# Optimization experiments

Measured on AMD Instinct MI355X. Metric: run time of the kernel, lower is better.

Reference implementation:

```python
import jax, jax.numpy as jnp
import numpy as np

N = 100_000   # nodes
E = 1_600_000 # edges (avg degree 16)
D = 64        # in_channel == out_channel (residual requires equality)
EPS = 1e-5    # BatchNorm1d eps


def setup_inputs() -> dict:
    key = jax.random.key(0)
    ks = jax.random.split(key, 8)
    x = jax.random.normal(ks[0], (N, D), dtype=jnp.float32)
    adj_val = jax.random.uniform(ks[1], (E,), dtype=jnp.float32) * 0.25  # sparse poly_adj values
    W = jax.random.normal(ks[2], (D, D), dtype=jnp.float32) / np.sqrt(D)  # Linear weight [out,in]
    b = jnp.zeros((D,), dtype=jnp.float32)
    gamma = jnp.ones((D,), dtype=jnp.float32)
    beta = jnp.zeros((D,), dtype=jnp.float32)
    adj_row = jax.random.randint(ks[3], (E,), 0, N, dtype=jnp.int32)
    adj_col = jax.random.randint(ks[4], (E,), 0, N, dtype=jnp.int32)
    return {"x": x, "adj_val": adj_val, "W": W, "b": b,
            "gamma": gamma, "beta": beta, "adj_row": adj_row, "adj_col": adj_col}


def reference(x, adj_val, W, b, gamma, beta, adj_row, adj_col):
    # h = poly_adj @ x  (COO SpMM via gather + segment_sum)
    h = jax.ops.segment_sum(adj_val[:, None] * x[adj_col], adj_row, num_segments=N)
    # Linear
    h = h @ W.T + b
    # residual
    h = h + x
    # BatchNorm1d (training-mode batch stats, biased variance)
    mean = jnp.mean(h, axis=0)
    var = jnp.mean(jnp.square(h - mean), axis=0)
    h = (h - mean) * jax.lax.rsqrt(var + EPS) * gamma + beta
    # ReLU (dropout with p=0 is identity)
    h = jax.nn.relu(h)
    return h
```

## Files before the change

### kernel.cpp

```cpp
#include <hip/hip_runtime.h>

#define DCH 64
#define BN_EPS 1e-5f

#define SUPSH 12
#define NSUPMAX 32
#define CAPS 67584
#define CHA 2048
#define CHB 2048
#define CPS 33
#define CAPF 1216
#define CITER 8

__device__ __forceinline__ unsigned bf16pair(float lo, float hi) {
    unsigned ul = (__float_as_uint(lo) + 0x8000u) >> 16;
    unsigned uh = (__float_as_uint(hi) + 0x8000u) & 0xffff0000u;
    return ul | uh;
}
__device__ __forceinline__ float bf_lo(unsigned u) { return __uint_as_float(u << 16); }
__device__ __forceinline__ float bf_hi(unsigned u) { return __uint_as_float(u & 0xffff0000u); }

__global__ __launch_bounds__(256) void gemm_xwt(const float* __restrict__ x,
                                                const float* __restrict__ W,
                                                unsigned short* __restrict__ yb,
                                                int* __restrict__ cursA,
                                                int* __restrict__ cursB,
                                                float* __restrict__ stats,
                                                int N) {
    const int tid = threadIdx.x;
    if (blockIdx.x == 0) {
        for (int i = tid; i < 2048; i += 256) cursB[i] = i * CAPF;
    } else if (blockIdx.x == 1) {
        if (tid < 128) stats[tid] = 0.f;
        if (tid < NSUPMAX) cursA[tid] = tid * CAPS;
    }

    __shared__ float xs[128 * 68];
    __shared__ float wt[64 * 64];
    const int blockRow = blockIdx.x * 128;

#pragma unroll
    for (int jj = 0; jj < 4; ++jj) {
        int idx4 = tid * 16 + jj * 4;
        int o = idx4 >> 6, k = idx4 & 63;
        float4 w4 = *(const float4*)&W[idx4];
        wt[(k + 0) * 64 + o] = w4.x;
        wt[(k + 1) * 64 + o] = w4.y;
        wt[(k + 2) * 64 + o] = w4.z;
        wt[(k + 3) * 64 + o] = w4.w;
    }
#pragma unroll
    for (int jj = 0; jj < 8; ++jj) {
        int f4 = tid + 256 * jj;
        int rl = f4 >> 4, k4 = (f4 & 15) * 4;
        int row = blockRow + rl;
        float4 v = make_float4(0.f, 0.f, 0.f, 0.f);
        if (row < N) v = *(const float4*)&x[row * DCH + k4];
        *(float4*)&xs[rl * 68 + k4] = v;
    }
    __syncthreads();

    const int tc = tid & 7;
    const int tr = tid >> 3;
    const int dc = tc * 8;
    float acc[4][8];
#pragma unroll
    for (int i = 0; i < 4; ++i)
#pragma unroll
        for (int j = 0; j < 8; ++j) acc[i][j] = 0.f;

    for (int k4 = 0; k4 < 16; ++k4) {
        float4 xv[4];
#pragma unroll
        for (int i = 0; i < 4; ++i)
            xv[i] = *(const float4*)&xs[(tr + 32 * i) * 68 + k4 * 4];
#pragma unroll
        for (int kk = 0; kk < 4; ++kk) {
            int k = k4 * 4 + kk;
            float4 w0 = *(const float4*)&wt[k * 64 + dc];
            float4 w1 = *(const float4*)&wt[k * 64 + dc + 4];
#pragma unroll
            for (int i = 0; i < 4; ++i) {
                float xvi = (kk == 0) ? xv[i].x : (kk == 1) ? xv[i].y
                           : (kk == 2) ? xv[i].z : xv[i].w;
                acc[i][0] = fmaf(xvi, w0.x, acc[i][0]);
                acc[i][1] = fmaf(xvi, w0.y, acc[i][1]);
                acc[i][2] = fmaf(xvi, w0.z, acc[i][2]);
                acc[i][3] = fmaf(xvi, w0.w, acc[i][3]);
                acc[i][4] = fmaf(xvi, w1.x, acc[i][4]);
                acc[i][5] = fmaf(xvi, w1.y, acc[i][5]);
                acc[i][6] = fmaf(xvi, w1.z, acc[i][6]);
                acc[i][7] = fmaf(xvi, w1.w, acc[i][7]);
            }
        }
    }
#pragma unroll
    for (int i = 0; i < 4; ++i) {
        int row = blockRow + tr + 32 * i;
        if (row < N) {
            uint4 p;
            p.x = bf16pair(acc[i][0], acc[i][1]);
            p.y = bf16pair(acc[i][2], acc[i][3]);
            p.z = bf16pair(acc[i][4], acc[i][5]);
            p.w = bf16pair(acc[i][6], acc[i][7]);
            *(uint4*)&yb[row * DCH + dc] = p;
        }
    }
}

__global__ __launch_bounds__(256) void bin_coarse(const int* __restrict__ rows,
                                                  const int* __restrict__ cols,
                                                  const float* __restrict__ vals,
                                                  int* __restrict__ cursA,
                                                  int2* __restrict__ edgesA,
                                                  int E, int NSUP) {
    __shared__ int2 stage[CHA];
    __shared__ unsigned char bOf[CHA];
    __shared__ int wc[32 * NSUPMAX];
    __shared__ int startB[NSUPMAX], totB[NSUPMAX], gbase[NSUPMAX];
    const int tid = threadIdx.x, lane = tid & 63, wave = tid >> 6;
    const int base = blockIdx.x * CHA;
    const int cnt = min(CHA, E - base);

    for (int i = tid; i < 32 * NSUPMAX; i += 256) wc[i] = 0;
    __syncthreads();

    int myr[CITER], myrank[CITER];
#pragma unroll
    for (int it = 0; it < CITER; ++it) {
        int k = tid + it * 256;
        bool act = k < cnt;
        int r = act ? rows[base + k] : 0;
        myr[it] = r;
        int key = r >> SUPSH;
        unsigned long long m = __ballot(act);
#pragma unroll
        for (int bit = 0; bit < 5; ++bit) {
            unsigned long long bb = __ballot((key >> bit) & 1);
            m &= ((key >> bit) & 1) ? bb : ~bb;
        }
        int rk = __popcll(m & ((1ULL << lane) - 1ULL));
        myrank[it] = rk;
        if (act && rk == 0) wc[(wave * CITER + it) * NSUPMAX + key] = __popcll(m);
    }
    __syncthreads();
    if (tid < NSUP) {
        int run = 0;
        for (int sub = 0; sub < 32; ++sub) {
            int t = wc[sub * NSUPMAX + tid];
            wc[sub * NSUPMAX + tid] = run;
            run += t;
        }
        totB[tid] = run;
    }
    __syncthreads();
    if (wave == 0) {
        int v = (lane < NSUP) ? totB[lane] : 0;
        int inc = v;
#pragma unroll
        for (int off = 1; off < 32; off <<= 1) {
            int u = __shfl_up(inc, off);
            if (lane >= off) inc += u;
        }
        if (lane < NSUP) {
            startB[lane] = inc - v;
            gbase[lane] = v ? atomicAdd(&cursA[lane], v) : 0;
        }
    }
    __syncthreads();
#pragma unroll
    for (int it = 0; it < CITER; ++it) {
        int k = tid + it * 256;
        if (k < cnt) {
            int r = myr[it];
            int key = r >> SUPSH;
            int pos = startB[key] + wc[(wave * CITER + it) * NSUPMAX + key] + myrank[it];
            int2 pk;
            pk.x = cols[base + k] | ((r & 4095) << 17);
            pk.y = __float_as_int(vals[base + k]);
            stage[pos] = pk;
            bOf[pos] = (unsigned char)key;
        }
    }
    __syncthreads();
#pragma unroll
    for (int it = 0; it < CITER; ++it) {
        int i = tid + it * 256;
        if (i < cnt) {
            int s = bOf[i];
            int pos = gbase[s] + (i - startB[s]);
            if (pos < (s + 1) * CAPS) edgesA[pos] = stage[i];
        }
    }
}

__global__ __launch_bounds__(256) void bin_fine(const int2* __restrict__ edgesA,
                                                const int* __restrict__ cursA,
                                                int* __restrict__ cursB,
                                                int2* __restrict__ edgesB) {
    __shared__ int2 stage[CHB];
    __shared__ unsigned char bOf[CHB];
    __shared__ int wc[32 * 64];
    __shared__ int startB[64], totB[64], gbase[64];
    const int tid = threadIdx.x, lane = tid & 63, wave = tid >> 6;
    const int s = blockIdx.x / CPS;
    const int c = blockIdx.x % CPS;
    const int base = s * CAPS + c * CHB;
    int fill = min(cursA[s] - s * CAPS, CAPS);
    int cnt = fill - c * CHB;
    cnt = max(0, min(CHB, cnt));

    for (int i = tid; i < 32 * 64; i += 256) wc[i] = 0;
    __syncthreads();

    int2 mypk[CITER];
    int myrank[CITER];
#pragma unroll
    for (int it = 0; it < CITER; ++it) {
        int k = tid + it * 256;
        bool act = k < cnt;
        int2 p = act ? edgesA[base + k] : make_int2(0, 0);
        mypk[it] = p;
        int key = (p.x >> 23) & 63;
        unsigned long long m = __ballot(act);
#pragma unroll
        for (int bit = 0; bit < 6; ++bit) {
            unsigned long long bb = __ballot((key >> bit) & 1);
            m &= ((key >> bit) & 1) ? bb : ~bb;
        }
        int rk = __popcll(m & ((1ULL << lane) - 1ULL));
        myrank[it] = rk;
        if (act && rk == 0) wc[(wave * CITER + it) * 64 + key] = __popcll(m);
    }
    __syncthreads();
    if (tid < 64) {
        int run = 0;
        for (int sub = 0; sub < 32; ++sub) {
            int t = wc[sub * 64 + tid];
            wc[sub * 64 + tid] = run;
            run += t;
        }
        totB[tid] = run;
    }
    __syncthreads();
    if (wave == 0) {
        int v = totB[lane];
        int inc = v;
#pragma unroll
        for (int off = 1; off < 64; off <<= 1) {
            int u = __shfl_up(inc, off);
            if (lane >= off) inc += u;
        }
        startB[lane] = inc - v;
        gbase[lane] = v ? atomicAdd(&cursB[s * 64 + lane], v) : 0;
    }
    __syncthreads();
#pragma unroll
    for (int it = 0; it < CITER; ++it) {
        int k = tid + it * 256;
        if (k < cnt) {
            int2 p = mypk[it];
            int key = (p.x >> 23) & 63;
            int pos = startB[key] + wc[(wave * CITER + it) * 64 + key] + myrank[it];
            stage[pos] = p;
            bOf[pos] = (unsigned char)key;
        }
    }
    __syncthreads();
#pragma unroll
    for (int it = 0; it < CITER; ++it) {
        int i = tid + it * 256;
        if (i < cnt) {
            int f = bOf[i];
            int gf = s * 64 + f;
            int pos = gbase[f] + (i - startB[f]);
            if (pos < (gf + 1) * CAPF) edgesB[pos] = stage[i];
        }
    }
}

#define SITER 5
__global__ __launch_bounds__(256) void spmm_sorted(const unsigned short* __restrict__ yb,
                                                   const int* __restrict__ cursB,
                                                   const int2* __restrict__ edges,
                                                   const float* __restrict__ x,
                                                   const float* __restrict__ bias,
                                                   unsigned short* __restrict__ zb,
                                                   float* __restrict__ stats, int N) {
    __shared__ int2 cv[CAPF];
    __shared__ int wc[4 * SITER * 64];
    __shared__ int startR[64], totR[64];
    __shared__ float rs[4][64];
    __shared__ float rs2[4][64];

    const int tid = threadIdx.x;
    const int b = blockIdx.x;
    const int beg = b * CAPF;
    int cnt = cursB[b] - beg;
    if (cnt > CAPF) cnt = CAPF;
    const int g = tid >> 3;
    const int q8 = tid & 7;
    const int wave = tid >> 6;
    const int lane = tid & 63;
    const int rowBase = b << 6;

    float bs[8];
    *(float4*)&bs[0] = *(const float4*)&bias[q8 * 8];
    *(float4*)&bs[4] = *(const float4*)&bias[q8 * 8 + 4];
    float s[8], s2[8];
#pragma unroll
    for (int i = 0; i < 8; ++i) { s[i] = 0.f; s2[i] = 0.f; }

    for (int i = tid; i < 4 * SITER * 64; i += 256) wc[i] = 0;
    __syncthreads();

    int2 mypk[SITER];
    int myrank[SITER];
#pragma unroll
    for (int it = 0; it < SITER; ++it) {
        int k = tid + it * 256;
        bool act = k < cnt;
        int2 p = act ? edges[beg + k] : make_int2(0, 0);
        mypk[it] = p;
        int key = (p.x >> 17) & 63;
        unsigned long long m = __ballot(act);
#pragma unroll
        for (int bit = 0; bit < 6; ++bit) {
            unsigned long long bb = __ballot((key >> bit) & 1);
            m &= ((key >> bit) & 1) ? bb : ~bb;
        }
        int rk = __popcll(m & ((1ULL << lane) - 1ULL));
        myrank[it] = rk;
        if (act && rk == 0) wc[(wave * SITER + it) * 64 + key] = __popcll(m);
    }
    __syncthreads();
    if (tid < 64) {
        int run = 0;
        for (int sub = 0; sub < 4 * SITER; ++sub) {
            int t = wc[sub * 64 + tid];
            wc[sub * 64 + tid] = run;
            run += t;
        }
        totR[tid] = run;
    }
    __syncthreads();
    if (wave == 0) {
        int v = totR[lane];
        int inc = v;
#pragma unroll
        for (int off = 1; off < 64; off <<= 1) {
            int u = __shfl_up(inc, off);
            if (lane >= off) inc += u;
        }
        startR[lane] = inc - v;
    }
    __syncthreads();
#pragma unroll
    for (int it = 0; it < SITER; ++it) {
        int k = tid + it * 256;
        if (k < cnt) {
            int2 p = mypk[it];
            int key = (p.x >> 17) & 63;
            int pos = startR[key] + wc[(wave * SITER + it) * 64 + key] + myrank[it];
            int2 pc;
            pc.x = p.x & 0x1ffff;
            pc.y = p.y;
            cv[pos] = pc;
        }
    }
    __syncthreads();

#pragma unroll
    for (int rr = 0; rr < 2; ++rr) {
        int lr = g * 2 + rr;
        int r = rowBase + lr;
        if (r >= N) break;
        int e0 = startR[lr];
        int e1 = e0 + totR[lr];
        float a[8];
#pragma unroll
        for (int i = 0; i < 8; ++i) a[i] = 0.f;
        for (int j = e0; j < e1; j += 4) {
            int cc[4]; float vv[4]; uint4 yq[4];
#pragma unroll
            for (int u = 0; u < 4; ++u) {
                bool ok = (j + u) < e1;
                int2 pc = cv[ok ? (j + u) : e0];
                cc[u] = pc.x;
                vv[u] = ok ? __int_as_float(pc.y) : 0.f;
            }
#pragma unroll
            for (int u = 0; u < 4; ++u)
                yq[u] = *(const uint4*)&yb[cc[u] * DCH + q8 * 8];
#pragma unroll
            for (int u = 0; u < 4; ++u) {
                a[0] = fmaf(vv[u], bf_lo(yq[u].x), a[0]);
                a[1] = fmaf(vv[u], bf_hi(yq[u].x), a[1]);
                a[2] = fmaf(vv[u], bf_lo(yq[u].y), a[2]);
                a[3] = fmaf(vv[u], bf_hi(yq[u].y), a[3]);
                a[4] = fmaf(vv[u], bf_lo(yq[u].z), a[4]);
                a[5] = fmaf(vv[u], bf_hi(yq[u].z), a[5]);
                a[6] = fmaf(vv[u], bf_lo(yq[u].w), a[6]);
                a[7] = fmaf(vv[u], bf_hi(yq[u].w), a[7]);
            }
        }
        float xv[8];
        *(float4*)&xv[0] = *(const float4*)&x[r * DCH + q8 * 8];
        *(float4*)&xv[4] = *(const float4*)&x[r * DCH + q8 * 8 + 4];
        float z[8];
#pragma unroll
        for (int i = 0; i < 8; ++i) {
            z[i] = a[i] + bs[i] + xv[i];
            s[i] += z[i];
            s2[i] = fmaf(z[i], z[i], s2[i]);
        }
        uint4 pz;
        pz.x = bf16pair(z[0], z[1]);
        pz.y = bf16pair(z[2], z[3]);
        pz.z = bf16pair(z[4], z[5]);
        pz.w = bf16pair(z[6], z[7]);
        *(uint4*)&zb[r * DCH + q8 * 8] = pz;
    }

#pragma unroll
    for (int m = 8; m <= 32; m <<= 1) {
#pragma unroll
        for (int i = 0; i < 8; ++i) {
            s[i] += __shfl_xor(s[i], m);
            s2[i] += __shfl_xor(s2[i], m);
        }
    }
    if (lane < 8) {
        *(float4*)&rs[wave][q8 * 8]      = *(float4*)&s[0];
        *(float4*)&rs[wave][q8 * 8 + 4]  = *(float4*)&s[4];
        *(float4*)&rs2[wave][q8 * 8]     = *(float4*)&s2[0];
        *(float4*)&rs2[wave][q8 * 8 + 4] = *(float4*)&s2[4];
    }
    __syncthreads();
    if (tid < 64) {
        float ts  = rs[0][tid] + rs[1][tid] + rs[2][tid] + rs[3][tid];
        float ts2 = rs2[0][tid] + rs2[1][tid] + rs2[2][tid] + rs2[3][tid];
        atomicAdd(&stats[tid], ts);
        atomicAdd(&stats[64 + tid], ts2);
    }
}

__global__ __launch_bounds__(256) void bn_relu(const unsigned short* __restrict__ zb,
                                               float* __restrict__ out,
                                               const float* __restrict__ stats,
                                               const float* __restrict__ gamma,
                                               const float* __restrict__ beta,
                                               int ND8, float invN) {
    const int tid = threadIdx.x;
    const int idx0 = blockIdx.x * 256 + tid;
    const int q8 = idx0 & 7;
    float sc[8], sh[8];
#pragma unroll
    for (int i = 0; i < 8; ++i) {
        int d = q8 * 8 + i;
        float mean = stats[d] * invN;
        float var = stats[64 + d] * invN - mean * mean;
        sc[i] = gamma[d] * rsqrtf(var + BN_EPS);
        sh[i] = beta[d] - mean * sc[i];
    }
    const int stride = gridDim.x * 256;
    for (int i = idx0; i < ND8; i += stride) {
        uint4 zq = *(const uint4*)&zb[i * 8];
        float z[8];
        z[0] = bf_lo(zq.x); z[1] = bf_hi(zq.x);
        z[2] = bf_lo(zq.y); z[3] = bf_hi(zq.y);
        z[4] = bf_lo(zq.z); z[5] = bf_hi(zq.z);
        z[6] = bf_lo(zq.w); z[7] = bf_hi(zq.w);
        float4 o0, o1;
        o0.x = fmaxf(fmaf(z[0], sc[0], sh[0]), 0.f);
        o0.y = fmaxf(fmaf(z[1], sc[1], sh[1]), 0.f);
        o0.z = fmaxf(fmaf(z[2], sc[2], sh[2]), 0.f);
        o0.w = fmaxf(fmaf(z[3], sc[3], sh[3]), 0.f);
        o1.x = fmaxf(fmaf(z[4], sc[4], sh[4]), 0.f);
        o1.y = fmaxf(fmaf(z[5], sc[5], sh[5]), 0.f);
        o1.z = fmaxf(fmaf(z[6], sc[6], sh[6]), 0.f);
        o1.w = fmaxf(fmaf(z[7], sc[7], sh[7]), 0.f);
        *(float4*)&out[i * 8] = o0;
        *(float4*)&out[i * 8 + 4] = o1;
    }
}

extern "C" void kernel_launch(void* const* d_in, const int* in_sizes, int n_in,
                              void* d_out, int out_size, void* d_ws, size_t ws_size,
                              hipStream_t stream) {
    const float* x       = (const float*)d_in[0];
    const float* adj_val = (const float*)d_in[1];
    const float* W       = (const float*)d_in[2];
    const float* b       = (const float*)d_in[3];
    const float* gamma   = (const float*)d_in[4];
    const float* beta    = (const float*)d_in[5];
    const int*   adj_row = (const int*)d_in[6];
    const int*   adj_col = (const int*)d_in[7];
    float* out = (float*)d_out;

    const int N  = in_sizes[0] / DCH;
    const int E  = in_sizes[1];
    const int ND = N * DCH;
    const int NSUP = (N + (1 << SUPSH) - 1) >> SUPSH;
    const int NFB  = NSUP * 64;

    char* ws = (char*)d_ws;
    size_t off = 0;
    float* stats = (float*)(ws + off); off += 512;
    int* cursA   = (int*)(ws + off);   off += NSUPMAX * 4;
    int* cursB   = (int*)(ws + off);   off += 2048 * 4;
    off = (off + 127) & ~127ull;
    unsigned short* yb = (unsigned short*)(ws + off); off += (size_t)ND * 2;
    off = (off + 127) & ~127ull;
    unsigned short* zb = (unsigned short*)(ws + off); off += (size_t)ND * 2;
    off = (off + 127) & ~127ull;
    int2* edgesA = (int2*)(ws + off);  off += (size_t)NSUP * CAPS * 8;
    int2* edgesB = (int2*)(ws + off);  off += (size_t)NFB * CAPF * 8;

    gemm_xwt<<<(N + 127) / 128, 256, 0, stream>>>(x, W, yb, cursA, cursB, stats, N);
    bin_coarse<<<(E + CHA - 1) / CHA, 256, 0, stream>>>(adj_row, adj_col, adj_val,
                                                        cursA, edgesA, E, NSUP);
    bin_fine<<<NSUP * CPS, 256, 0, stream>>>(edgesA, cursA, cursB, edgesB);
    spmm_sorted<<<NFB, 256, 0, stream>>>(yb, cursB, edgesB, x, b, zb, stats, N);
    bn_relu<<<1024, 256, 0, stream>>>(zb, out, stats, gamma, beta, ND / 8,
                                      1.0f / (float)N);
}
```

Before: 215.1 us.

## Fuse GEMM with coarse binning, use LDS atomics for ranks, spread BN stats atomics

The GEMM and the coarse edge binning now run in one launch, with even and odd blocks taking the two roles. The ballot-based ranking in all three binning stages is replaced by shared-memory atomic histograms, which removes the per-wave count arrays and their scans. SpMM now gives each 8-thread group two consecutive rows and unrolls the gather by 8, and BN statistics are spread over 8 replicas to reduce global atomic contention; bn_relu reduces the replicas once per block into shared memory. Cursors are now relative offsets cleared by a memset, which adds an extra launch, and LDS atomics give nondeterministic edge order within a bin.

```diff
diff --git a/kernel.cpp b/kernel.cpp
--- a/kernel.cpp
+++ b/kernel.cpp
@@ -11,6 +11,7 @@
 #define CPS 33
 #define CAPF 1216
 #define CITER 8
+#define SITER 5
 
 __device__ __forceinline__ unsigned bf16pair(float lo, float hi) {
     unsigned ul = (__float_as_uint(lo) + 0x8000u) >> 16;
@@ -20,176 +21,158 @@
 __device__ __forceinline__ float bf_lo(unsigned u) { return __uint_as_float(u << 16); }
 __device__ __forceinline__ float bf_hi(unsigned u) { return __uint_as_float(u & 0xffff0000u); }
 
-__global__ __launch_bounds__(256) void gemm_xwt(const float* __restrict__ x,
+__global__ __launch_bounds__(256) void gemm_bin(const float* __restrict__ x,
                                                 const float* __restrict__ W,
                                                 unsigned short* __restrict__ yb,
+                                                const int* __restrict__ rows,
+                                                const int* __restrict__ cols,
+                                                const float* __restrict__ vals,
                                                 int* __restrict__ cursA,
-                                                int* __restrict__ cursB,
-                                                float* __restrict__ stats,
-                                                int N) {
+                                                int2* __restrict__ edgesA,
+                                                int N, int E, int GB, int BB,
+                                                int NSUP) {
+    __shared__ __align__(16) char smem[51200];
     const int tid = threadIdx.x;
-    if (blockIdx.x == 0) {
-        for (int i = tid; i < 2048; i += 256) cursB[i] = i * CAPF;
-    } else if (blockIdx.x == 1) {
-        if (tid < 128) stats[tid] = 0.f;
-        if (tid < NSUPMAX) cursA[tid] = tid * CAPS;
-    }
-
-    __shared__ float xs[128 * 68];
-    __shared__ float wt[64 * 64];
-    const int blockRow = blockIdx.x * 128;
-
-#pragma unroll
-    for (int jj = 0; jj < 4; ++jj) {
-        int idx4 = tid * 16 + jj * 4;
-        int o = idx4 >> 6, k = idx4 & 63;
-        float4 w4 = *(const float4*)&W[idx4];
-        wt[(k + 0) * 64 + o] = w4.x;
-        wt[(k + 1) * 64 + o] = w4.y;
-        wt[(k + 2) * 64 + o] = w4.z;
-        wt[(k + 3) * 64 + o] = w4.w;
-    }
-#pragma unroll
-    for (int jj = 0; jj < 8; ++jj) {
-        int f4 = tid + 256 * jj;
-        int rl = f4 >> 4, k4 = (f4 & 15) * 4;
-        int row = blockRow + rl;
-        float4 v = make_float4(0.f, 0.f, 0.f, 0.f);
-        if (row < N) v = *(const float4*)&x[row * DCH + k4];
-        *(float4*)&xs[rl * 68 + k4] = v;
-    }
-    __syncthreads();
-
-    const int tc = tid & 7;
-    const int tr = tid >> 3;
-    const int dc = tc * 8;
-    float acc[4][8];
-#pragma unroll
-    for (int i = 0; i < 4; ++i)
-#pragma unroll
-        for (int j = 0; j < 8; ++j) acc[i][j] = 0.f;
-
-    for (int k4 = 0; k4 < 16; ++k4) {
-        float4 xv[4];
+    const int role = blockIdx.x & 1;
+    const int idx = blockIdx.x >> 1;
+
+    if (role == 0) {
+        if (idx >= GB) return;
+        float* xs = (float*)smem;
+        float* wt = (float*)(smem + 34816);
+        const int blockRow = idx * 128;
+
+#pragma unroll
+        for (int jj = 0; jj < 4; ++jj) {
+            int idx4 = tid * 16 + jj * 4;
+            int o = idx4 >> 6, k = idx4 & 63;
+            float4 w4 = *(const float4*)&W[idx4];
+            wt[(k + 0) * 64 + o] = w4.x;
+            wt[(k + 1) * 64 + o] = w4.y;
+            wt[(k + 2) * 64 + o] = w4.z;
+            wt[(k + 3) * 64 + o] = w4.w;
+        }
+#pragma unroll
+        for (int jj = 0; jj < 8; ++jj) {
+            int f4 = tid + 256 * jj;
+            int rl = f4 >> 4, k4 = (f4 & 15) * 4;
+            int row = blockRow + rl;
+            float4 v = make_float4(0.f, 0.f, 0.f, 0.f);
+            if (row < N) v = *(const float4*)&x[row * DCH + k4];
+            *(float4*)&xs[rl * 68 + k4] = v;
+        }
+        __syncthreads();
+
+        const int tc = tid & 7;
+        const int tr = tid >> 3;
+        const int dc = tc * 8;
+        float acc[4][8];
 #pragma unroll
         for (int i = 0; i < 4; ++i)
-            xv[i] = *(const float4*)&xs[(tr + 32 * i) * 68 + k4 * 4];
-#pragma unroll
-        for (int kk = 0; kk < 4; ++kk) {
-            int k = k4 * 4 + kk;
-            float4 w0 = *(const float4*)&wt[k * 64 + dc];
-            float4 w1 = *(const float4*)&wt[k * 64 + dc + 4];
-#pragma unroll
-            for (int i = 0; i < 4; ++i) {
-                float xvi = (kk == 0) ? xv[i].x : (kk == 1) ? xv[i].y
-                           : (kk == 2) ? xv[i].z : xv[i].w;
-                acc[i][0] = fmaf(xvi, w0.x, acc[i][0]);
-                acc[i][1] = fmaf(xvi, w0.y, acc[i][1]);
-                acc[i][2] = fmaf(xvi, w0.z, acc[i][2]);
-                acc[i][3] = fmaf(xvi, w0.w, acc[i][3]);
-                acc[i][4] = fmaf(xvi, w1.x, acc[i][4]);
-                acc[i][5] = fmaf(xvi, w1.y, acc[i][5]);
-                acc[i][6] = fmaf(xvi, w1.z, acc[i][6]);
-                acc[i][7] = fmaf(xvi, w1.w, acc[i][7]);
-            }
-        }
-    }
-#pragma unroll
-    for (int i = 0; i < 4; ++i) {
-        int row = blockRow + tr + 32 * i;
-        if (row < N) {
-            uint4 p;
-            p.x = bf16pair(acc[i][0], acc[i][1]);
-            p.y = bf16pair(acc[i][2], acc[i][3]);
-            p.z = bf16pair(acc[i][4], acc[i][5]);
-            p.w = bf16pair(acc[i][6], acc[i][7]);
-            *(uint4*)&yb[row * DCH + dc] = p;
-        }
-    }
-}
-
-__global__ __launch_bounds__(256) void bin_coarse(const int* __restrict__ rows,
-                                                  const int* __restrict__ cols,
-                                                  const float* __restrict__ vals,
-                                                  int* __restrict__ cursA,
-                                                  int2* __restrict__ edgesA,
-                                                  int E, int NSUP) {
-    __shared__ int2 stage[CHA];
-    __shared__ unsigned char bOf[CHA];
-    __shared__ int wc[32 * NSUPMAX];
-    __shared__ int startB[NSUPMAX], totB[NSUPMAX], gbase[NSUPMAX];
-    const int tid = threadIdx.x, lane = tid & 63, wave = tid >> 6;
-    const int base = blockIdx.x * CHA;
-    const int cnt = min(CHA, E - base);
-
-    for (int i = tid; i < 32 * NSUPMAX; i += 256) wc[i] = 0;
-    __syncthreads();
-
-    int myr[CITER], myrank[CITER];
-#pragma unroll
-    for (int it = 0; it < CITER; ++it) {
-        int k = tid + it * 256;
-        bool act = k < cnt;
-        int r = act ? rows[base + k] : 0;
-        myr[it] = r;
-        int key = r >> SUPSH;
-        unsigned long long m = __ballot(act);
-#pragma unroll
-        for (int bit = 0; bit < 5; ++bit) {
-            unsigned long long bb = __ballot((key >> bit) & 1);
-            m &= ((key >> bit) & 1) ? bb : ~bb;
-        }
-        int rk = __popcll(m & ((1ULL << lane) - 1ULL));
-        myrank[it] = rk;
-        if (act && rk == 0) wc[(wave * CITER + it) * NSUPMAX + key] = __popcll(m);
-    }
-    __syncthreads();
-    if (tid < NSUP) {
-        int run = 0;
-        for (int sub = 0; sub < 32; ++sub) {
-            int t = wc[sub * NSUPMAX + tid];
-            wc[sub * NSUPMAX + tid] = run;
-            run += t;
-        }
-        totB[tid] = run;
-    }
-    __syncthreads();
-    if (wave == 0) {
-        int v = (lane < NSUP) ? totB[lane] : 0;
-        int inc = v;
-#pragma unroll
-        for (int off = 1; off < 32; off <<= 1) {
-            int u = __shfl_up(inc, off);
-            if (lane >= off) inc += u;
-        }
-        if (lane < NSUP) {
-            startB[lane] = inc - v;
-            gbase[lane] = v ? atomicAdd(&cursA[lane], v) : 0;
-        }
-    }
-    __syncthreads();
-#pragma unroll
-    for (int it = 0; it < CITER; ++it) {
-        int k = tid + it * 256;
-        if (k < cnt) {
-            int r = myr[it];
-            int key = r >> SUPSH;
-            int pos = startB[key] + wc[(wave * CITER + it) * NSUPMAX + key] + myrank[it];
-            int2 pk;
-            pk.x = cols[base + k] | ((r & 4095) << 17);
-            pk.y = __float_as_int(vals[base + k]);
-            stage[pos] = pk;
-            bOf[pos] = (unsigned char)key;
-        }
-    }
-    __syncthreads();
-#pragma unroll
-    for (int it = 0; it < CITER; ++it) {
-        int i = tid + it * 256;
-        if (i < cnt) {
-            int s = bOf[i];
-            int pos = gbase[s] + (i - startB[s]);
-            if (pos < (s + 1) * CAPS) edgesA[pos] = stage[i];
+#pragma unroll
+            for (int j = 0; j < 8; ++j) acc[i][j] = 0.f;
+
+        for (int k4 = 0; k4 < 16; ++k4) {
+            float4 xv[4];
+#pragma unroll
+            for (int i = 0; i < 4; ++i)
+                xv[i] = *(const float4*)&xs[(tr + 32 * i) * 68 + k4 * 4];
+#pragma unroll
+            for (int kk = 0; kk < 4; ++kk) {
+                int k = k4 * 4 + kk;
+                float4 w0 = *(const float4*)&wt[k * 64 + dc];
+                float4 w1 = *(const float4*)&wt[k * 64 + dc + 4];
+#pragma unroll
+                for (int i = 0; i < 4; ++i) {
+                    float xvi = (kk == 0) ? xv[i].x : (kk == 1) ? xv[i].y
+                               : (kk == 2) ? xv[i].z : xv[i].w;
+                    acc[i][0] = fmaf(xvi, w0.x, acc[i][0]);
+                    acc[i][1] = fmaf(xvi, w0.y, acc[i][1]);
+                    acc[i][2] = fmaf(xvi, w0.z, acc[i][2]);
+                    acc[i][3] = fmaf(xvi, w0.w, acc[i][3]);
+                    acc[i][4] = fmaf(xvi, w1.x, acc[i][4]);
+                    acc[i][5] = fmaf(xvi, w1.y, acc[i][5]);
+                    acc[i][6] = fmaf(xvi, w1.z, acc[i][6]);
+                    acc[i][7] = fmaf(xvi, w1.w, acc[i][7]);
+                }
+            }
+        }
+#pragma unroll
+        for (int i = 0; i < 4; ++i) {
+            int row = blockRow + tr + 32 * i;
+            if (row < N) {
+                uint4 p;
+                p.x = bf16pair(acc[i][0], acc[i][1]);
+                p.y = bf16pair(acc[i][2], acc[i][3]);
+                p.z = bf16pair(acc[i][4], acc[i][5]);
+                p.w = bf16pair(acc[i][6], acc[i][7]);
+                *(uint4*)&yb[row * DCH + dc] = p;
+            }
+        }
+    } else {
+        if (idx >= BB) return;
+        int2* stage = (int2*)smem;
+        unsigned char* bOf = (unsigned char*)(smem + 16384);
+        int* hist   = (int*)(smem + 18432);
+        int* startB = (int*)(smem + 18560);
+        int* gbase  = (int*)(smem + 18688);
+        const int lane = tid & 63, wave = tid >> 6;
+        const int base = idx * CHA;
+        const int cnt = min(CHA, E - base);
+
+        for (int i = tid; i < NSUPMAX; i += 256) hist[i] = 0;
+        __syncthreads();
+
+        int myr[CITER], mycol[CITER], myrank[CITER];
+        float myv[CITER];
+#pragma unroll
+        for (int it = 0; it < CITER; ++it) {
+            int k = tid + it * 256;
+            if (k < cnt) {
+                int r = rows[base + k];
+                myr[it] = r;
+                mycol[it] = cols[base + k];
+                myv[it] = vals[base + k];
+                myrank[it] = atomicAdd(&hist[r >> SUPSH], 1);
+            }
+        }
+        __syncthreads();
+        if (wave == 0) {
+            int v = (lane < NSUP) ? hist[lane] : 0;
+            int inc = v;
+#pragma unroll
+            for (int off = 1; off < 32; off <<= 1) {
+                int u = __shfl_up(inc, off);
+                if (lane >= off) inc += u;
+            }
+            if (lane < NSUP) {
+                startB[lane] = inc - v;
+                gbase[lane] = v ? atomicAdd(&cursA[lane], v) : 0;
+            }
+        }
+        __syncthreads();
+#pragma unroll
+        for (int it = 0; it < CITER; ++it) {
+            int k = tid + it * 256;
+            if (k < cnt) {
+                int key = myr[it] >> SUPSH;
+                int pos = startB[key] + myrank[it];
+                int2 pk;
+                pk.x = mycol[it] | ((myr[it] & 4095) << 17);
+                pk.y = __float_as_int(myv[it]);
+                stage[pos] = pk;
+                bOf[pos] = (unsigned char)key;
+            }
+        }
+        __syncthreads();
+#pragma unroll
+        for (int it = 0; it < CITER; ++it) {
+            int i = tid + it * 256;
+            if (i < cnt) {
+                int s = bOf[i];
+                int rel = gbase[s] + (i - startB[s]);
+                if (rel < CAPS) edgesA[s * CAPS + rel] = stage[i];
+            }
         }
     }
 }
@@ -200,17 +183,15 @@
                                                 int2* __restrict__ edgesB) {
     __shared__ int2 stage[CHB];
     __shared__ unsigned char bOf[CHB];
-    __shared__ int wc[32 * 64];
-    __shared__ int startB[64], totB[64], gbase[64];
+    __shared__ int hist[64], startB[64], gbase[64];
     const int tid = threadIdx.x, lane = tid & 63, wave = tid >> 6;
     const int s = blockIdx.x / CPS;
     const int c = blockIdx.x % CPS;
     const int base = s * CAPS + c * CHB;
-    int fill = min(cursA[s] - s * CAPS, CAPS);
-    int cnt = fill - c * CHB;
-    cnt = max(0, min(CHB, cnt));
-
-    for (int i = tid; i < 32 * 64; i += 256) wc[i] = 0;
+    int fill = min(cursA[s], CAPS);
+    int cnt = max(0, min(CHB, fill - c * CHB));
+
+    for (int i = tid; i < 64; i += 256) hist[i] = 0;
     __syncthreads();
 
     int2 mypk[CITER];
@@ -218,33 +199,15 @@
 #pragma unroll
     for (int it = 0; it < CITER; ++it) {
         int k = tid + it * 256;
-        bool act = k < cnt;
-        int2 p = act ? edgesA[base + k] : make_int2(0, 0);
-        mypk[it] = p;
-        int key = (p.x >> 23) & 63;
-        unsigned long long m = __ballot(act);
-#pragma unroll
-        for (int bit = 0; bit < 6; ++bit) {
-            unsigned long long bb = __ballot((key >> bit) & 1);
-            m &= ((key >> bit) & 1) ? bb : ~bb;
-        }
-        int rk = __popcll(m & ((1ULL << lane) - 1ULL));
-        myrank[it] = rk;
-        if (act && rk == 0) wc[(wave * CITER + it) * 64 + key] = __popcll(m);
-    }
-    __syncthreads();
-    if (tid < 64) {
-        int run = 0;
-        for (int sub = 0; sub < 32; ++sub) {
-            int t = wc[sub * 64 + tid];
-            wc[sub * 64 + tid] = run;
-            run += t;
-        }
-        totB[tid] = run;
+        if (k < cnt) {
+            int2 p = edgesA[base + k];
+            mypk[it] = p;
+            myrank[it] = atomicAdd(&hist[(p.x >> 23) & 63], 1);
+        }
     }
     __syncthreads();
     if (wave == 0) {
-        int v = totB[lane];
+        int v = hist[lane];
         int inc = v;
 #pragma unroll
         for (int off = 1; off < 64; off <<= 1) {
@@ -261,7 +224,7 @@
         if (k < cnt) {
             int2 p = mypk[it];
             int key = (p.x >> 23) & 63;
-            int pos = startB[key] + wc[(wave * CITER + it) * 64 + key] + myrank[it];
+            int pos = startB[key] + myrank[it];
             stage[pos] = p;
             bOf[pos] = (unsigned char)key;
         }
@@ -272,14 +235,12 @@
         int i = tid + it * 256;
         if (i < cnt) {
             int f = bOf[i];
-            int gf = s * 64 + f;
-            int pos = gbase[f] + (i - startB[f]);
-            if (pos < (gf + 1) * CAPF) edgesB[pos] = stage[i];
+            int rel = gbase[f] + (i - startB[f]);
+            if (rel < CAPF) edgesB[(s * 64 + f) * CAPF + rel] = stage[i];
         }
     }
 }
 
-#define SITER 5
 __global__ __launch_bounds__(256) void spmm_sorted(const unsigned short* __restrict__ yb,
                                                    const int* __restrict__ cursB,
                                                    const int2* __restrict__ edges,
@@ -288,30 +249,22 @@
                                                    unsigned short* __restrict__ zb,
                                                    float* __restrict__ stats, int N) {
     __shared__ int2 cv[CAPF];
-    __shared__ int wc[4 * SITER * 64];
-    __shared__ int startR[64], totR[64];
+    __shared__ int hist[64];
+    __shared__ int startE[66];
     __shared__ float rs[4][64];
     __shared__ float rs2[4][64];
 
     const int tid = threadIdx.x;
     const int b = blockIdx.x;
     const int beg = b * CAPF;
-    int cnt = cursB[b] - beg;
-    if (cnt > CAPF) cnt = CAPF;
+    int cnt = min(cursB[b], CAPF);
     const int g = tid >> 3;
     const int q8 = tid & 7;
     const int wave = tid >> 6;
     const int lane = tid & 63;
     const int rowBase = b << 6;
 
-    float bs[8];
-    *(float4*)&bs[0] = *(const float4*)&bias[q8 * 8];
-    *(float4*)&bs[4] = *(const float4*)&bias[q8 * 8 + 4];
-    float s[8], s2[8];
-#pragma unroll
-    for (int i = 0; i < 8; ++i) { s[i] = 0.f; s2[i] = 0.f; }
-
-    for (int i = tid; i < 4 * SITER * 64; i += 256) wc[i] = 0;
+    for (int i = tid; i < 64; i += 256) hist[i] = 0;
     __syncthreads();
 
     int2 mypk[SITER];
@@ -319,40 +272,23 @@
 #pragma unroll
     for (int it = 0; it < SITER; ++it) {
         int k = tid + it * 256;
-        bool act = k < cnt;
-        int2 p = act ? edges[beg + k] : make_int2(0, 0);
-        mypk[it] = p;
-        int key = (p.x >> 17) & 63;
-        unsigned long long m = __ballot(act);
-#pragma unroll
-        for (int bit = 0; bit < 6; ++bit) {
-            unsigned long long bb = __ballot((key >> bit) & 1);
-            m &= ((key >> bit) & 1) ? bb : ~bb;
-        }
-        int rk = __popcll(m & ((1ULL << lane) - 1ULL));
-        myrank[it] = rk;
-        if (act && rk == 0) wc[(wave * SITER + it) * 64 + key] = __popcll(m);
-    }
-    __syncthreads();
-    if (tid < 64) {
-        int run = 0;
-        for (int sub = 0; sub < 4 * SITER; ++sub) {
-            int t = wc[sub * 64 + tid];
-            wc[sub * 64 + tid] = run;
-            run += t;
-        }
-        totR[tid] = run;
+        if (k < cnt) {
+            int2 p = edges[beg + k];
+            mypk[it] = p;
+            myrank[it] = atomicAdd(&hist[(p.x >> 17) & 63], 1);
+        }
     }
     __syncthreads();
     if (wave == 0) {
-        int v = totR[lane];
+        int v = hist[lane];
         int inc = v;
 #pragma unroll
         for (int off = 1; off < 64; off <<= 1) {
             int u = __shfl_up(inc, off);
             if (lane >= off) inc += u;
         }
-        startR[lane] = inc - v;
+        startE[lane] = inc - v;
+        if (lane == 63) startE[64] = inc;
     }
     __syncthreads();
 #pragma unroll
@@ -361,66 +297,90 @@
         if (k < cnt) {
             int2 p = mypk[it];
             int key = (p.x >> 17) & 63;
-            int pos = startR[key] + wc[(wave * SITER + it) * 64 + key] + myrank[it];
             int2 pc;
             pc.x = p.x & 0x1ffff;
             pc.y = p.y;
-            cv[pos] = pc;
-        }
-    }
-    __syncthreads();
-
-#pragma unroll
-    for (int rr = 0; rr < 2; ++rr) {
-        int lr = g * 2 + rr;
-        int r = rowBase + lr;
-        if (r >= N) break;
-        int e0 = startR[lr];
-        int e1 = e0 + totR[lr];
-        float a[8];
-#pragma unroll
-        for (int i = 0; i < 8; ++i) a[i] = 0.f;
-        for (int j = e0; j < e1; j += 4) {
-            int cc[4]; float vv[4]; uint4 yq[4];
-#pragma unroll
-            for (int u = 0; u < 4; ++u) {
-                bool ok = (j + u) < e1;
-                int2 pc = cv[ok ? (j + u) : e0];
-                cc[u] = pc.x;
-                vv[u] = ok ? __int_as_float(pc.y) : 0.f;
-            }
-#pragma unroll
-            for (int u = 0; u < 4; ++u)
-                yq[u] = *(const uint4*)&yb[cc[u] * DCH + q8 * 8];
-#pragma unroll
-            for (int u = 0; u < 4; ++u) {
-                a[0] = fmaf(vv[u], bf_lo(yq[u].x), a[0]);
-                a[1] = fmaf(vv[u], bf_hi(yq[u].x), a[1]);
-                a[2] = fmaf(vv[u], bf_lo(yq[u].y), a[2]);
-                a[3] = fmaf(vv[u], bf_hi(yq[u].y), a[3]);
-                a[4] = fmaf(vv[u], bf_lo(yq[u].z), a[4]);
-                a[5] = fmaf(vv[u], bf_hi(yq[u].z), a[5]);
-                a[6] = fmaf(vv[u], bf_lo(yq[u].w), a[6]);
-                a[7] = fmaf(vv[u], bf_hi(yq[u].w), a[7]);
-            }
-        }
-        float xv[8];
-        *(float4*)&xv[0] = *(const float4*)&x[r * DCH + q8 * 8];
-        *(float4*)&xv[4] = *(const float4*)&x[r * DCH + q8 * 8 + 4];
-        float z[8];
-#pragma unroll
-        for (int i = 0; i < 8; ++i) {
-            z[i] = a[i] + bs[i] + xv[i];
-            s[i] += z[i];
-            s2[i] = fmaf(z[i], z[i], s2[i]);
-        }
-        uint4 pz;
-        pz.x = bf16pair(z[0], z[1]);
-        pz.y = bf16pair(z[2], z[3]);
-        pz.z = bf16pair(z[4], z[5]);
-        pz.w = bf16pair(z[6], z[7]);
-        *(uint4*)&zb[r * DCH + q8 * 8] = pz;
-    }
+            cv[startE[key] + myrank[it]] = pc;
+        }
+    }
+    __syncthreads();
+
+    float bs[8];
+    *(float4*)&bs[0] = *(const float4*)&bias[q8 * 8];
+    *(float4*)&bs[4] = *(const float4*)&bias[q8 * 8 + 4];
+
+    const int lr0 = g * 2;
+    const int e0 = startE[lr0];
+    const int split = startE[lr0 + 1];
+    const int e1 = startE[lr0 + 2];
+    float a0[8], a1[8];
+#pragma unroll
+    for (int i = 0; i < 8; ++i) { a0[i] = 0.f; a1[i] = 0.f; }
+
+    for (int j = e0; j < e1; j += 8) {
+        int cc[8];
+        float v0[8], v1[8];
+#pragma unroll
+        for (int u = 0; u < 8; ++u) {
+            int idx = j + u;
+            bool ok = idx < e1;
+            int2 pc = cv[ok ? idx : e0];
+            float v = ok ? __int_as_float(pc.y) : 0.f;
+            bool sec = idx >= split;
+            v0[u] = sec ? 0.f : v;
+            v1[u] = sec ? v : 0.f;
+            cc[u] = pc.x;
+        }
+        uint4 yq[8];
+#pragma unroll
+        for (int u = 0; u < 8; ++u)
+            yq[u] = *(const uint4*)&yb[cc[u] * DCH + q8 * 8];
+#pragma unroll
+        for (int u = 0; u < 8; ++u) {
+            float t0 = bf_lo(yq[u].x), t1 = bf_hi(yq[u].x);
+            a0[0] = fmaf(v0[u], t0, a0[0]); a1[0] = fmaf(v1[u], t0, a1[0]);
+            a0[1] = fmaf(v0[u], t1, a0[1]); a1[1] = fmaf(v1[u], t1, a1[1]);
+            t0 = bf_lo(yq[u].y); t1 = bf_hi(yq[u].y);
+            a0[2] = fmaf(v0[u], t0, a0[2]); a1[2] = fmaf(v1[u], t0, a1[2]);
+            a0[3] = fmaf(v0[u], t1, a0[3]); a1[3] = fmaf(v1[u], t1, a1[3]);
+            t0 = bf_lo(yq[u].z); t1 = bf_hi(yq[u].z);
+            a0[4] = fmaf(v0[u], t0, a0[4]); a1[4] = fmaf(v1[u], t0, a1[4]);
+            a0[5] = fmaf(v0[u], t1, a0[5]); a1[5] = fmaf(v1[u], t1, a1[5]);
+            t0 = bf_lo(yq[u].w); t1 = bf_hi(yq[u].w);
+            a0[6] = fmaf(v0[u], t0, a0[6]); a1[6] = fmaf(v1[u], t0, a1[6]);
+            a0[7] = fmaf(v0[u], t1, a0[7]); a1[7] = fmaf(v1[u], t1, a1[7]);
+        }
+    }
+
+    float s[8], s2[8];
+#pragma unroll
+    for (int i = 0; i < 8; ++i) { s[i] = 0.f; s2[i] = 0.f; }
+
+#define EMIT(A, LR)                                                         \
+    {                                                                       \
+        int r = rowBase + (LR);                                             \
+        if (r < N) {                                                        \
+            float xv[8];                                                    \
+            *(float4*)&xv[0] = *(const float4*)&x[r * DCH + q8 * 8];        \
+            *(float4*)&xv[4] = *(const float4*)&x[r * DCH + q8 * 8 + 4];    \
+            float z[8];                                                     \
+            _Pragma("unroll")                                               \
+            for (int i = 0; i < 8; ++i) {                                   \
+                z[i] = A[i] + bs[i] + xv[i];                                \
+                s[i] += z[i];                                               \
+                s2[i] = fmaf(z[i], z[i], s2[i]);                            \
+            }                                                               \
+            uint4 pz;                                                       \
+            pz.x = bf16pair(z[0], z[1]);                                    \
+            pz.y = bf16pair(z[2], z[3]);                                    \
+            pz.z = bf16pair(z[4], z[5]);                                    \
+            pz.w = bf16pair(z[6], z[7]);                                    \
+            *(uint4*)&zb[r * DCH + q8 * 8] = pz;                            \
+        }                                                                   \
+    }
+    EMIT(a0, lr0)
+    EMIT(a1, lr0 + 1)
+#undef EMIT
 
 #pragma unroll
     for (int m = 8; m <= 32; m <<= 1) {
@@ -440,8 +400,9 @@
     if (tid < 64) {
         float ts  = rs[0][tid] + rs[1][tid] + rs[2][tid] + rs[3][tid];
         float ts2 = rs2[0][tid] + rs2[1][tid] + rs2[2][tid] + rs2[3][tid];
-        atomicAdd(&stats[tid], ts);
-        atomicAdd(&stats[64 + tid], ts2);
+        float* st = stats + ((b & 7) << 7);
+        atomicAdd(&st[tid], ts);
+        atomicAdd(&st[64 + tid], ts2);
     }
 }
 
@@ -451,17 +412,30 @@
                                                const float* __restrict__ gamma,
                                                const float* __restrict__ beta,
                                                int ND8, float invN) {
+    __shared__ float lsc[64], lsh[64];
     const int tid = threadIdx.x;
+    if (tid < 64) {
+        float s = 0.f, s2 = 0.f;
+#pragma unroll
+        for (int r = 0; r < 8; ++r) {
+            s  += stats[r * 128 + tid];
+            s2 += stats[r * 128 + 64 + tid];
+        }
+        float mean = s * invN;
+        float var = s2 * invN - mean * mean;
+        float sc = gamma[tid] * rsqrtf(var + BN_EPS);
+        lsc[tid] = sc;
+        lsh[tid] = beta[tid] - mean * sc;
+    }
+    __syncthreads();
+
     const int idx0 = blockIdx.x * 256 + tid;
     const int q8 = idx0 & 7;
     float sc[8], sh[8];
 #pragma unroll
     for (int i = 0; i < 8; ++i) {
-        int d = q8 * 8 + i;
-        float mean = stats[d] * invN;
-        float var = stats[64 + d] * invN - mean * mean;
-        sc[i] = gamma[d] * rsqrtf(var + BN_EPS);
-        sh[i] = beta[d] - mean * sc[i];
+        sc[i] = lsc[q8 * 8 + i];
+        sh[i] = lsh[q8 * 8 + i];
     }
     const int stride = gridDim.x * 256;
     for (int i = idx0; i < ND8; i += stride) {
@@ -505,11 +479,10 @@
     const int NFB  = NSUP * 64;
 
     char* ws = (char*)d_ws;
-    size_t off = 0;
-    float* stats = (float*)(ws + off); off += 512;
-    int* cursA   = (int*)(ws + off);   off += NSUPMAX * 4;
-    int* cursB   = (int*)(ws + off);   off += 2048 * 4;
-    off = (off + 127) & ~127ull;
+    float* stats = (float*)ws;
+    int* cursA   = (int*)(ws + 4096);
+    int* cursB   = (int*)(ws + 4224);
+    size_t off = 12416;
     unsigned short* yb = (unsigned short*)(ws + off); off += (size_t)ND * 2;
     off = (off + 127) & ~127ull;
     unsigned short* zb = (unsigned short*)(ws + off); off += (size_t)ND * 2;
@@ -517,9 +490,14 @@
     int2* edgesA = (int2*)(ws + off);  off += (size_t)NSUP * CAPS * 8;
     int2* edgesB = (int2*)(ws + off);  off += (size_t)NFB * CAPF * 8;
 
-    gemm_xwt<<<(N + 127) / 128, 256, 0, stream>>>(x, W, yb, cursA, cursB, stats, N);
-    bin_coarse<<<(E + CHA - 1) / CHA, 256, 0, stream>>>(adj_row, adj_col, adj_val,
-                                                        cursA, edgesA, E, NSUP);
+    hipMemsetAsync(ws, 0, 12416, stream);
+
+    const int GB = (N + 127) / 128;
+    const int BB = (E + CHA - 1) / CHA;
+    const int PAIRS = (GB > BB) ? GB : BB;
+
+    gemm_bin<<<2 * PAIRS, 256, 0, stream>>>(x, W, yb, adj_row, adj_col, adj_val,
+                                            cursA, edgesA, N, E, GB, BB, NSUP);
     bin_fine<<<NSUP * CPS, 256, 0, stream>>>(edgesA, cursA, cursB, edgesB);
     spmm_sorted<<<NFB, 256, 0, stream>>>(yb, cursB, edgesB, x, b, zb, stats, N);
     bn_relu<<<1024, 256, 0, stream>>>(zb, out, stats, gamma, beta, ND / 8,
```

Measured after the change: 175.6 us. 1.22x faster.
